# Optimization experiments

Hardware: AMD Instinct MI355X
Metric: run time of the kernel (lower is better)

Reference implementation:

```python
import jax, jax.numpy as jnp
import numpy as np

N_HOPS = 3
GAMMA = 0.2
N_CAP = 3  # self.N: hops < N use alpha, hop == N uses eta
EPS = 1e-8

N_USERS, N_ENT, N_KG_EDGES, N_INTER_EDGES, D, N_REL = 50000, 100000, 300000, 300000, 256, 21


def setup_inputs() -> dict:
    key = jax.random.key(0)
    ks = jax.random.split(key, 9)
    user_emb = jax.random.normal(ks[0], (N_USERS, D), jnp.float32) * 0.1
    entity_emb = jax.random.normal(ks[1], (N_ENT, D), jnp.float32) * 0.1
    edge_index = jax.random.randint(ks[2], (2, N_KG_EDGES), 0, N_ENT, dtype=jnp.int32)
    edge_type = jax.random.randint(ks[3], (N_KG_EDGES,), 1, N_REL, dtype=jnp.int32)  # 1-based relation ids
    omega = jax.random.uniform(ks[4], (N_KG_EDGES,), jnp.float32)
    inter_u = jax.random.randint(ks[5], (N_INTER_EDGES,), 0, N_USERS, dtype=jnp.int32)
    inter_i = jax.random.randint(ks[6], (N_INTER_EDGES,), 0, N_ENT, dtype=jnp.int32)
    inter_edge = jnp.stack([inter_u, inter_i])
    inter_edge_w = jax.random.uniform(ks[7], (N_INTER_EDGES,), jnp.float32)
    relation_emb = jax.random.normal(ks[8], (N_REL - 1, D), jnp.float32) * 0.1  # xavier-like
    return {
        "user_emb": user_emb,
        "entity_emb": entity_emb,
        "edge_index": edge_index,
        "edge_type": edge_type,
        "omega": omega,
        "inter_edge": inter_edge,
        "inter_edge_w": inter_edge_w,
        "relation_emb": relation_emb,
    }


def _l2norm(x):
    # F.normalize(x, dim=-1, eps=1e-8): x / max(||x||_2, eps)
    n = jnp.sqrt(jnp.sum(x * x, axis=-1, keepdims=True))
    return x / jnp.maximum(n, EPS)


def _clean(x):
    return jnp.nan_to_num(x, nan=0.0, posinf=10000.0, neginf=0.0001)


def reference(user_emb, entity_emb, edge_index, edge_type, omega, inter_edge, inter_edge_w, relation_emb):
    head, tail = edge_index[0], edge_index[1]
    E = omega.shape[0]
    n_ent = entity_emb.shape[0]
    n_users = user_emb.shape[0]

    # alpha/eta depend only on omega & head (constant across hops) -> hoist out of the hop loop
    denom = jax.ops.segment_sum(omega, head, num_segments=E)[head] + EPS
    alpha = omega / denom
    eta0 = jnp.where(alpha > GAMMA, alpha, 0.0)
    eta = eta0 / (jax.ops.segment_sum(eta0, head, num_segments=E)[head] + EPS)

    rel = relation_emb[edge_type - 1]  # [E, D]
    cnt = jnp.maximum(jax.ops.segment_sum(jnp.ones((E,), entity_emb.dtype), head, num_segments=n_ent), 1.0)

    ent_res, usr_res = entity_emb, user_emb
    ent, usr = entity_emb, user_emb
    for i in range(N_HOPS):
        hop = i + 1
        rho = alpha if hop < N_CAP else eta
        msg = rho[:, None] * (ent[tail] * rel)                       # [E, D]
        ent_agg = jax.ops.segment_sum(msg, head, num_segments=n_ent) / cnt[:, None]  # scatter_mean
        item_agg = inter_edge_w[:, None] * ent[inter_edge[1]]        # [IE, D]
        usr_agg = jax.ops.segment_sum(item_agg, inter_edge[0], num_segments=n_users)  # scatter_sum
        ent = _clean(_l2norm(ent_agg))
        usr = _clean(_l2norm(usr_agg))
        ent_res = ent_res + ent
        usr_res = usr_res + usr
    return (ent_res, usr_res)
```

## Files before the change

### kernel.cpp

```cpp
#include <hip/hip_runtime.h>
#include <math.h>

#define D 256
#define EPSV 1e-8f
#define GAMMAV 0.2f
#define SCAN_B 256

__device__ __forceinline__ float cleanf(float x) {
    if (isnan(x)) return 0.0f;
    if (isinf(x)) return x > 0.0f ? 10000.0f : 0.0001f;
    return x;
}

__device__ __forceinline__ unsigned short f2bf(float x) {
    unsigned u = __float_as_uint(x);
    return (unsigned short)((u + 0x7FFFu + ((u >> 16) & 1u)) >> 16);
}
__device__ __forceinline__ float bf2f(unsigned short b) {
    return __uint_as_float(((unsigned)b) << 16);
}


__global__ __launch_bounds__(256) void k_pre(
    const float4* __restrict__ ein, ushort4* __restrict__ eout, int n4, int nbc,
    const int* __restrict__ head, const float* __restrict__ omega,
    const int* __restrict__ iu,
    int* __restrict__ counts_e, int* __restrict__ counts_u,
    float* __restrict__ denom, int E, int IE) {
    if ((int)blockIdx.x < nbc) {
        int i = blockIdx.x * 256 + threadIdx.x;
        if (i < n4) {
            float4 v = ein[i];
            eout[i] = make_ushort4(f2bf(v.x), f2bf(v.y), f2bf(v.z), f2bf(v.w));
        }
    } else {
        int i = (blockIdx.x - nbc) * 256 + threadIdx.x;
        if (i < E) {
            int h = head[i];
            atomicAdd(&counts_e[h], 1);
            atomicAdd(&denom[h], omega[i]);
        } else if (i < E + IE) {
            atomicAdd(&counts_u[iu[i - E]], 1);
        }
    }
}


__global__ __launch_bounds__(SCAN_B) void k_scan1(
    const int* __restrict__ ce, int* __restrict__ oe, int* __restrict__ be,
    int nE, int nbE,
    const int* __restrict__ cu, int* __restrict__ ou, int* __restrict__ bu,
    int nU) {
    __shared__ int tmp[SCAN_B];
    const int* in; int* out; int* bs; int n; int lb;
    if ((int)blockIdx.x < nbE) { in = ce; out = oe; bs = be; n = nE; lb = blockIdx.x; }
    else { in = cu; out = ou; bs = bu; n = nU; lb = blockIdx.x - nbE; }
    int i = lb * SCAN_B + threadIdx.x;
    int v = (i < n) ? in[i] : 0;
    tmp[threadIdx.x] = v;
    __syncthreads();
    for (int o = 1; o < SCAN_B; o <<= 1) {
        int t = (threadIdx.x >= (unsigned)o) ? tmp[threadIdx.x - o] : 0;
        __syncthreads();
        tmp[threadIdx.x] += t;
        __syncthreads();
    }
    if (i < n) out[i] = tmp[threadIdx.x] - v;
    if (threadIdx.x == SCAN_B - 1) bs[lb] = tmp[threadIdx.x];
}

__global__ __launch_bounds__(1024) void k_scan2(
    int* __restrict__ be, int nbE, int* __restrict__ bu, int nbU) {
    __shared__ int tmp[1024];
    int* bs = (blockIdx.x == 0) ? be : bu;
    int nb  = (blockIdx.x == 0) ? nbE : nbU;
    int v = ((int)threadIdx.x < nb) ? bs[threadIdx.x] : 0;
    tmp[threadIdx.x] = v;
    __syncthreads();
    for (int o = 1; o < 1024; o <<= 1) {
        int t = (threadIdx.x >= (unsigned)o) ? tmp[threadIdx.x - o] : 0;
        __syncthreads();
        tmp[threadIdx.x] += t;
        __syncthreads();
    }
    if ((int)threadIdx.x < nb) bs[threadIdx.x] = tmp[threadIdx.x] - v;
}

__global__ __launch_bounds__(SCAN_B) void k_scan3(
    int* __restrict__ oe, int* __restrict__ cure, const int* __restrict__ be,
    int nE, int nbE,
    int* __restrict__ ou, int* __restrict__ curu, const int* __restrict__ bu,
    int nU) {
    int* out; int* cur; const int* bs; int n; int lb;
    if ((int)blockIdx.x < nbE) { out = oe; cur = cure; bs = be; n = nE; lb = blockIdx.x; }
    else { out = ou; cur = curu; bs = bu; n = nU; lb = blockIdx.x - nbE; }
    int i = lb * SCAN_B + threadIdx.x;
    if (i < n) {
        int v = out[i] + bs[lb];
        out[i] = v;
        cur[i] = v;
    }
}


__global__ __launch_bounds__(256) void k_fill_both(
    const int* __restrict__ head, const int* __restrict__ tail,
    const int* __restrict__ etype, const float* __restrict__ omega,
    const int* __restrict__ iu, const int* __restrict__ ii,
    const float* __restrict__ iw,
    const float* __restrict__ denom, float* __restrict__ denom2,
    int* __restrict__ cursor_e, int* __restrict__ cursor_u,
    int2* __restrict__ kg, int2* __restrict__ uc, int E, int IE) {
    int i = blockIdx.x * blockDim.x + threadIdx.x;
    if (i < E) {
        int h = head[i];
        float a = omega[i] / (denom[h] + EPSV);
        int p = atomicAdd(&cursor_e[h], 1);
        int2 m;
        m.x = tail[i] | ((etype[i] - 1) << 20);
        m.y = __float_as_int(a);
        kg[p] = m;
        if (a > GAMMAV) atomicAdd(&denom2[h], a);
    } else if (i < E + IE) {
        int e = i - E;
        int u = iu[e];
        int p = atomicAdd(&cursor_u[u], 1);
        int2 m;
        m.x = ii[e];
        m.y = __float_as_int(iw[e]);
        uc[p] = m;
    }
}


__global__ __launch_bounds__(256) void k_hop(
    const int* __restrict__ offs_e, const int* __restrict__ cnt_e,
    const int2* __restrict__ kg,
    const int* __restrict__ offs_u, const int* __restrict__ cnt_u,
    const int2* __restrict__ uc,
    const float* __restrict__ denom2,
    const float* __restrict__ rel,
    const unsigned short* __restrict__ src,
    const unsigned short* __restrict__ ent0b,
    const unsigned short* __restrict__ y1b,
    const unsigned short* __restrict__ y2b,
    unsigned short* __restrict__ ent_out_b,
    float* __restrict__ ent_res,
    const float* __restrict__ user0,
    float* __restrict__ usr_res,
    int n_ent, int n_users, int hop) {
    int row  = (int)((blockIdx.x * (size_t)blockDim.x + threadIdx.x) >> 6);
    int lane = threadIdx.x & 63;
    if (row < n_ent) {
        int s = offs_e[row], deg = cnt_e[row];
        int end = s + deg;
        const bool eta = (hop == 3);
        float den2i = 0.0f;
        if (eta) den2i = 1.0f / (denom2[row] + EPSV);
        float4 acc = make_float4(0.f, 0.f, 0.f, 0.f);
        for (int j = s; j < end; j += 4) {
            int e1 = end - 1;
            int2 mm[4];
            #pragma unroll
            for (int k = 0; k < 4; ++k) {
                int jj = j + k;
                mm[k] = kg[jj < end ? jj : e1];
            }
            ushort4 eb[4];
            float4  rw[4];
            float   rv[4];
            #pragma unroll
            for (int k = 0; k < 4; ++k) {
                int t = mm[k].x & 0xFFFFF;
                int r = ((unsigned)mm[k].x) >> 20;
                float a = __int_as_float(mm[k].y);
                float x = a;
                if (eta) x = (a > GAMMAV) ? a * den2i : 0.0f;
                rv[k] = (j + k < end) ? x : 0.0f;
                eb[k] = ((const ushort4*)(src + (size_t)t * D))[lane];
                rw[k] = ((const float4*)(rel + (size_t)r * D))[lane];
            }
            #pragma unroll
            for (int k = 0; k < 4; ++k) {
                acc.x += rv[k] * bf2f(eb[k].x) * rw[k].x;
                acc.y += rv[k] * bf2f(eb[k].y) * rw[k].y;
                acc.z += rv[k] * bf2f(eb[k].z) * rw[k].z;
                acc.w += rv[k] * bf2f(eb[k].w) * rw[k].w;
            }
        }
        float cinv = 1.0f / ((deg > 0) ? (float)deg : 1.0f);
        acc.x *= cinv; acc.y *= cinv; acc.z *= cinv; acc.w *= cinv;
        float ss = acc.x * acc.x + acc.y * acc.y + acc.z * acc.z + acc.w * acc.w;
        #pragma unroll
        for (int o = 32; o >= 1; o >>= 1) ss += __shfl_down(ss, o);
        ss = __shfl(ss, 0);
        float nrm = sqrtf(ss);
        float dninv = 1.0f / ((nrm > EPSV) ? nrm : EPSV);
        float4 y;
        y.x = cleanf(acc.x * dninv);
        y.y = cleanf(acc.y * dninv);
        y.z = cleanf(acc.z * dninv);
        y.w = cleanf(acc.w * dninv);
        if (hop == 3) {
            ushort4 a0 = ((const ushort4*)(ent0b + (size_t)row * D))[lane];
            ushort4 a1 = ((const ushort4*)(y1b  + (size_t)row * D))[lane];
            ushort4 a2 = ((const ushort4*)(y2b  + (size_t)row * D))[lane];
            y.x += bf2f(a0.x) + bf2f(a1.x) + bf2f(a2.x);
            y.y += bf2f(a0.y) + bf2f(a1.y) + bf2f(a2.y);
            y.z += bf2f(a0.z) + bf2f(a1.z) + bf2f(a2.z);
            y.w += bf2f(a0.w) + bf2f(a1.w) + bf2f(a2.w);
            ((float4*)(ent_res + (size_t)row * D))[lane] = y;
        } else {
            ((ushort4*)(ent_out_b + (size_t)row * D))[lane] =
                make_ushort4(f2bf(y.x), f2bf(y.y), f2bf(y.z), f2bf(y.w));
        }
    } else {
        int u = row - n_ent;
        if (u >= n_users) return;
        int s = offs_u[u], deg = cnt_u[u];
        int end = s + deg;
        float4 acc = make_float4(0.f, 0.f, 0.f, 0.f);
        for (int j = s; j < end; j += 4) {
            int e1 = end - 1;
            int2 mm[4];
            #pragma unroll
            for (int k = 0; k < 4; ++k) {
                int jj = j + k;
                mm[k] = uc[jj < end ? jj : e1];
            }
            ushort4 eb[4];
            float   wv[4];
            #pragma unroll
            for (int k = 0; k < 4; ++k) {
                wv[k] = (j + k < end) ? __int_as_float(mm[k].y) : 0.0f;
                eb[k] = ((const ushort4*)(src + (size_t)mm[k].x * D))[lane];
            }
            #pragma unroll
            for (int k = 0; k < 4; ++k) {
                acc.x += wv[k] * bf2f(eb[k].x);
                acc.y += wv[k] * bf2f(eb[k].y);
                acc.z += wv[k] * bf2f(eb[k].z);
                acc.w += wv[k] * bf2f(eb[k].w);
            }
        }
        float ss = acc.x * acc.x + acc.y * acc.y + acc.z * acc.z + acc.w * acc.w;
        #pragma unroll
        for (int o = 32; o >= 1; o >>= 1) ss += __shfl_down(ss, o);
        ss = __shfl(ss, 0);
        float nrm = sqrtf(ss);
        float dninv = 1.0f / ((nrm > EPSV) ? nrm : EPSV);
        float4 y;
        y.x = cleanf(acc.x * dninv);
        y.y = cleanf(acc.y * dninv);
        y.z = cleanf(acc.z * dninv);
        y.w = cleanf(acc.w * dninv);
        float4 base;
        if (hop == 1) base = ((const float4*)(user0 + (size_t)u * D))[lane];
        else          base = ((const float4*)(usr_res + (size_t)u * D))[lane];
        y.x += base.x; y.y += base.y; y.z += base.z; y.w += base.w;
        ((float4*)(usr_res + (size_t)u * D))[lane] = y;
    }
}

extern "C" void kernel_launch(void* const* d_in, const int* in_sizes, int n_in,
                              void* d_out, int out_size, void* d_ws, size_t ws_size,
                              hipStream_t stream) {
    const float* user_emb   = (const float*)d_in[0];
    const float* entity_emb = (const float*)d_in[1];
    const int*   edge_index = (const int*)d_in[2];
    const int*   edge_type  = (const int*)d_in[3];
    const float* omega      = (const float*)d_in[4];
    const int*   inter_edge = (const int*)d_in[5];
    const float* inter_w    = (const float*)d_in[6];
    const float* rel_emb    = (const float*)d_in[7];

    const int n_users = in_sizes[0] / D;
    const int n_ent   = in_sizes[1] / D;
    const int E       = in_sizes[3];
    const int IE      = in_sizes[6];

    const int* head = edge_index;
    const int* tail = edge_index + E;
    const int* iu   = inter_edge;
    const int* ii   = inter_edge + IE;

    char* w = (char*)d_ws;
    size_t entBh = (size_t)n_ent * D * sizeof(unsigned short);
    unsigned short* ent0b = (unsigned short*)w;  w += entBh;
    unsigned short* ent_a = (unsigned short*)w;  w += entBh;
    unsigned short* ent_b = (unsigned short*)w;  w += entBh;
    int2*  kg    = (int2*)w;   w += (size_t)E * sizeof(int2);
    int2*  ucsr  = (int2*)w;   w += (size_t)IE * sizeof(int2);
    int*   counts_e = (int*)w;   w += (size_t)n_ent * sizeof(int);
    int*   counts_u = (int*)w;   w += (size_t)n_users * sizeof(int);
    float* denom    = (float*)w; w += (size_t)n_ent * sizeof(float);
    float* denom2   = (float*)w; w += (size_t)n_ent * sizeof(float);
    size_t zeroB = ((size_t)n_ent * 3 + n_users) * sizeof(int);
    int*   offs_e   = (int*)w; w += (size_t)n_ent * sizeof(int);
    int*   offs_u   = (int*)w; w += (size_t)n_users * sizeof(int);
    int*   cursor_e = (int*)w; w += (size_t)n_ent * sizeof(int);
    int*   cursor_u = (int*)w; w += (size_t)n_users * sizeof(int);
    int*   bsums_e  = (int*)w; w += 1024 * sizeof(int);
    int*   bsums_u  = (int*)w; w += 1024 * sizeof(int);

    float* ent_res = (float*)d_out;
    float* usr_res = (float*)d_out + (size_t)n_ent * D;

    hipMemsetAsync(counts_e, 0, zeroB, stream);

    int n4  = n_ent * (D / 4);
    int nbc = (n4 + 255) / 256;
    int total_edges = E + IE;
    int eb = (total_edges + 255) / 256;
    k_pre<<<nbc + eb, 256, 0, stream>>>(
        (const float4*)entity_emb, (ushort4*)ent0b, n4, nbc,
        head, omega, iu, counts_e, counts_u, denom, E, IE);

    int nbE = (n_ent + SCAN_B - 1) / SCAN_B;
    int nbU = (n_users + SCAN_B - 1) / SCAN_B;
    k_scan1<<<nbE + nbU, SCAN_B, 0, stream>>>(counts_e, offs_e, bsums_e, n_ent, nbE,
                                              counts_u, offs_u, bsums_u, n_users);
    k_scan2<<<2, 1024, 0, stream>>>(bsums_e, nbE, bsums_u, nbU);
    k_scan3<<<nbE + nbU, SCAN_B, 0, stream>>>(offs_e, cursor_e, bsums_e, n_ent, nbE,
                                              offs_u, cursor_u, bsums_u, n_users);

    k_fill_both<<<eb, 256, 0, stream>>>(head, tail, edge_type, omega, iu, ii,
                                        inter_w, denom, denom2,
                                        cursor_e, cursor_u, kg, ucsr, E, IE);

    size_t waves = (size_t)n_ent + n_users;
    int gb = (int)((waves * 64 + 255) / 256);

    k_hop<<<gb, 256, 0, stream>>>(offs_e, counts_e, kg, offs_u, counts_u, ucsr,
                                  denom2, rel_emb, ent0b, ent0b, ent_a, ent_b,
                                  ent_a, ent_res, user_emb, usr_res,
                                  n_ent, n_users, 1);
    k_hop<<<gb, 256, 0, stream>>>(offs_e, counts_e, kg, offs_u, counts_u, ucsr,
                                  denom2, rel_emb, ent_a, ent0b, ent_a, ent_b,
                                  ent_b, ent_res, user_emb, usr_res,
                                  n_ent, n_users, 2);
    k_hop<<<gb, 256, 0, stream>>>(offs_e, counts_e, kg, offs_u, counts_u, ucsr,
                                  denom2, rel_emb, ent_b, ent0b, ent_a, ent_b,
                                  ent_b , ent_res, user_emb, usr_res,
                                  n_ent, n_users, 3);
}
```

Before: 613.2 us.

## Merge scan kernels, pack CSR offset/count, and deepen gather loads in hop kernel

Replaces the three-kernel scan with one two-block scan kernel where each thread serially sums a contiguous chunk. Offsets and counts are packed into int2 so each row loads both with one access. In the hop kernel, residual and base loads are hoisted ahead of the gather loop, the user loop is unrolled to 8 gathers, and sched_barriers force all loads to issue before the FMAs. These aim to cut launch overhead and raise memory-level parallelism. The cost is a serial, poorly coalesced scan on only two blocks and higher register pressure.

Result: slower. 826.5 us (+34.8%).

```diff
diff --git a/kernel.cpp b/kernel.cpp
--- a/kernel.cpp
+++ b/kernel.cpp
@@ -4,7 +4,6 @@
 #define D 256
 #define EPSV 1e-8f
 #define GAMMAV 0.2f
-#define SCAN_B 256
 
 __device__ __forceinline__ float cleanf(float x) {
     if (isnan(x)) return 0.0f;
@@ -18,6 +17,24 @@
 }
 __device__ __forceinline__ float bf2f(unsigned short b) {
     return __uint_as_float(((unsigned)b) << 16);
+}
+
+__device__ __forceinline__ float ewgt(int bits, bool eta, float den2i) {
+    float a = __int_as_float(bits);
+    return eta ? ((a > GAMMAV) ? a * den2i : 0.0f) : a;
+}
+
+__device__ __forceinline__ void fma4(float4& acc, float w, ushort4 eb, float4 rw) {
+    acc.x += w * bf2f(eb.x) * rw.x;
+    acc.y += w * bf2f(eb.y) * rw.y;
+    acc.z += w * bf2f(eb.z) * rw.z;
+    acc.w += w * bf2f(eb.w) * rw.w;
+}
+__device__ __forceinline__ void fma4u(float4& acc, float w, ushort4 eb) {
+    acc.x += w * bf2f(eb.x);
+    acc.y += w * bf2f(eb.y);
+    acc.z += w * bf2f(eb.z);
+    acc.w += w * bf2f(eb.w);
 }
 
 
@@ -46,59 +63,33 @@
 }
 
 
-__global__ __launch_bounds__(SCAN_B) void k_scan1(
-    const int* __restrict__ ce, int* __restrict__ oe, int* __restrict__ be,
-    int nE, int nbE,
-    const int* __restrict__ cu, int* __restrict__ ou, int* __restrict__ bu,
-    int nU) {
-    __shared__ int tmp[SCAN_B];
-    const int* in; int* out; int* bs; int n; int lb;
-    if ((int)blockIdx.x < nbE) { in = ce; out = oe; bs = be; n = nE; lb = blockIdx.x; }
-    else { in = cu; out = ou; bs = bu; n = nU; lb = blockIdx.x - nbE; }
-    int i = lb * SCAN_B + threadIdx.x;
-    int v = (i < n) ? in[i] : 0;
-    tmp[threadIdx.x] = v;
-    __syncthreads();
-    for (int o = 1; o < SCAN_B; o <<= 1) {
-        int t = (threadIdx.x >= (unsigned)o) ? tmp[threadIdx.x - o] : 0;
-        __syncthreads();
-        tmp[threadIdx.x] += t;
-        __syncthreads();
-    }
-    if (i < n) out[i] = tmp[threadIdx.x] - v;
-    if (threadIdx.x == SCAN_B - 1) bs[lb] = tmp[threadIdx.x];
-}
-
-__global__ __launch_bounds__(1024) void k_scan2(
-    int* __restrict__ be, int nbE, int* __restrict__ bu, int nbU) {
+__global__ __launch_bounds__(1024) void k_scan(
+    const int* __restrict__ ce, int2* __restrict__ oce, int* __restrict__ cure, int nE,
+    const int* __restrict__ cu, int2* __restrict__ ocu, int* __restrict__ curu, int nU) {
+    const int* cnt; int2* oc; int* cur; int n;
+    if (blockIdx.x == 0) { cnt = ce; oc = oce; cur = cure; n = nE; }
+    else                 { cnt = cu; oc = ocu; cur = curu; n = nU; }
+    int per = (n + 1023) / 1024;
+    int t = threadIdx.x;
+    int s0 = t * per;
+    int s1 = s0 + per; if (s1 > n) s1 = n;
+    int sum = 0;
+    for (int i = s0; i < s1; ++i) sum += cnt[i];
     __shared__ int tmp[1024];
-    int* bs = (blockIdx.x == 0) ? be : bu;
-    int nb  = (blockIdx.x == 0) ? nbE : nbU;
-    int v = ((int)threadIdx.x < nb) ? bs[threadIdx.x] : 0;
-    tmp[threadIdx.x] = v;
+    tmp[t] = sum;
     __syncthreads();
     for (int o = 1; o < 1024; o <<= 1) {
-        int t = (threadIdx.x >= (unsigned)o) ? tmp[threadIdx.x - o] : 0;
+        int v = (t >= o) ? tmp[t - o] : 0;
         __syncthreads();
-        tmp[threadIdx.x] += t;
+        tmp[t] += v;
         __syncthreads();
     }
-    if ((int)threadIdx.x < nb) bs[threadIdx.x] = tmp[threadIdx.x] - v;
-}
-
-__global__ __launch_bounds__(SCAN_B) void k_scan3(
-    int* __restrict__ oe, int* __restrict__ cure, const int* __restrict__ be,
-    int nE, int nbE,
-    int* __restrict__ ou, int* __restrict__ curu, const int* __restrict__ bu,
-    int nU) {
-    int* out; int* cur; const int* bs; int n; int lb;
-    if ((int)blockIdx.x < nbE) { out = oe; cur = cure; bs = be; n = nE; lb = blockIdx.x; }
-    else { out = ou; cur = curu; bs = bu; n = nU; lb = blockIdx.x - nbE; }
-    int i = lb * SCAN_B + threadIdx.x;
-    if (i < n) {
-        int v = out[i] + bs[lb];
-        out[i] = v;
-        cur[i] = v;
+    int base = tmp[t] - sum;
+    for (int i = s0; i < s1; ++i) {
+        int c = cnt[i];
+        oc[i] = make_int2(base, c);
+        cur[i] = base;
+        base += c;
     }
 }
 
@@ -134,10 +125,8 @@
 
 
 __global__ __launch_bounds__(256) void k_hop(
-    const int* __restrict__ offs_e, const int* __restrict__ cnt_e,
-    const int2* __restrict__ kg,
-    const int* __restrict__ offs_u, const int* __restrict__ cnt_u,
-    const int2* __restrict__ uc,
+    const int2* __restrict__ oc_e, const int2* __restrict__ kg,
+    const int2* __restrict__ oc_u, const int2* __restrict__ uc,
     const float* __restrict__ denom2,
     const float* __restrict__ rel,
     const unsigned short* __restrict__ src,
@@ -151,42 +140,48 @@
     int n_ent, int n_users, int hop) {
     int row  = (int)((blockIdx.x * (size_t)blockDim.x + threadIdx.x) >> 6);
     int lane = threadIdx.x & 63;
+    const ushort4* srcv = (const ushort4*)src;
+    const float4*  relv = (const float4*)rel;
     if (row < n_ent) {
-        int s = offs_e[row], deg = cnt_e[row];
+        int2 oc = oc_e[row];
+        int s = oc.x, deg = oc.y;
         int end = s + deg;
         const bool eta = (hop == 3);
         float den2i = 0.0f;
-        if (eta) den2i = 1.0f / (denom2[row] + EPSV);
+        ushort4 a0, a1, a2;
+        if (eta) {
+            den2i = 1.0f / (denom2[row] + EPSV);
+            a0 = ((const ushort4*)ent0b)[row * 64 + lane];
+            a1 = ((const ushort4*)y1b )[row * 64 + lane];
+            a2 = ((const ushort4*)y2b )[row * 64 + lane];
+        }
         float4 acc = make_float4(0.f, 0.f, 0.f, 0.f);
         for (int j = s; j < end; j += 4) {
             int e1 = end - 1;
-            int2 mm[4];
-            #pragma unroll
-            for (int k = 0; k < 4; ++k) {
-                int jj = j + k;
-                mm[k] = kg[jj < end ? jj : e1];
-            }
-            ushort4 eb[4];
-            float4  rw[4];
-            float   rv[4];
-            #pragma unroll
-            for (int k = 0; k < 4; ++k) {
-                int t = mm[k].x & 0xFFFFF;
-                int r = ((unsigned)mm[k].x) >> 20;
-                float a = __int_as_float(mm[k].y);
-                float x = a;
-                if (eta) x = (a > GAMMAV) ? a * den2i : 0.0f;
-                rv[k] = (j + k < end) ? x : 0.0f;
-                eb[k] = ((const ushort4*)(src + (size_t)t * D))[lane];
-                rw[k] = ((const float4*)(rel + (size_t)r * D))[lane];
-            }
-            #pragma unroll
-            for (int k = 0; k < 4; ++k) {
-                acc.x += rv[k] * bf2f(eb[k].x) * rw[k].x;
-                acc.y += rv[k] * bf2f(eb[k].y) * rw[k].y;
-                acc.z += rv[k] * bf2f(eb[k].z) * rw[k].z;
-                acc.w += rv[k] * bf2f(eb[k].w) * rw[k].w;
-            }
+            int j1 = (j + 1 < end) ? j + 1 : e1;
+            int j2 = (j + 2 < end) ? j + 2 : e1;
+            int j3 = (j + 3 < end) ? j + 3 : e1;
+            int2 m0 = kg[j];
+            int2 m1 = kg[j1];
+            int2 m2 = kg[j2];
+            int2 m3 = kg[j3];
+            ushort4 eb0 = srcv[(m0.x & 0xFFFFF) * 64 + lane];
+            ushort4 eb1 = srcv[(m1.x & 0xFFFFF) * 64 + lane];
+            ushort4 eb2 = srcv[(m2.x & 0xFFFFF) * 64 + lane];
+            ushort4 eb3 = srcv[(m3.x & 0xFFFFF) * 64 + lane];
+            float4 rw0 = relv[(((unsigned)m0.x) >> 20) * 64 + lane];
+            float4 rw1 = relv[(((unsigned)m1.x) >> 20) * 64 + lane];
+            float4 rw2 = relv[(((unsigned)m2.x) >> 20) * 64 + lane];
+            float4 rw3 = relv[(((unsigned)m3.x) >> 20) * 64 + lane];
+            __builtin_amdgcn_sched_barrier(0);
+            float w0 = ewgt(m0.y, eta, den2i);
+            float w1 = (j + 1 < end) ? ewgt(m1.y, eta, den2i) : 0.0f;
+            float w2 = (j + 2 < end) ? ewgt(m2.y, eta, den2i) : 0.0f;
+            float w3 = (j + 3 < end) ? ewgt(m3.y, eta, den2i) : 0.0f;
+            fma4(acc, w0, eb0, rw0);
+            fma4(acc, w1, eb1, rw1);
+            fma4(acc, w2, eb2, rw2);
+            fma4(acc, w3, eb3, rw3);
         }
         float cinv = 1.0f / ((deg > 0) ? (float)deg : 1.0f);
         acc.x *= cinv; acc.y *= cinv; acc.z *= cinv; acc.w *= cinv;
@@ -202,9 +197,6 @@
         y.z = cleanf(acc.z * dninv);
         y.w = cleanf(acc.w * dninv);
         if (hop == 3) {
-            ushort4 a0 = ((const ushort4*)(ent0b + (size_t)row * D))[lane];
-            ushort4 a1 = ((const ushort4*)(y1b  + (size_t)row * D))[lane];
-            ushort4 a2 = ((const ushort4*)(y2b  + (size_t)row * D))[lane];
             y.x += bf2f(a0.x) + bf2f(a1.x) + bf2f(a2.x);
             y.y += bf2f(a0.y) + bf2f(a1.y) + bf2f(a2.y);
             y.z += bf2f(a0.z) + bf2f(a1.z) + bf2f(a2.z);
@@ -217,30 +209,30 @@
     } else {
         int u = row - n_ent;
         if (u >= n_users) return;
-        int s = offs_u[u], deg = cnt_u[u];
+        int2 oc = oc_u[u];
+        int s = oc.x, deg = oc.y;
         int end = s + deg;
+        float4 base;
+        if (hop == 1) base = ((const float4*)user0)[u * 64 + lane];
+        else          base = ((const float4*)usr_res)[u * 64 + lane];
         float4 acc = make_float4(0.f, 0.f, 0.f, 0.f);
-        for (int j = s; j < end; j += 4) {
+        for (int j = s; j < end; j += 8) {
             int e1 = end - 1;
-            int2 mm[4];
+            int2 mm[8];
             #pragma unroll
-            for (int k = 0; k < 4; ++k) {
+            for (int k = 0; k < 8; ++k) {
                 int jj = j + k;
                 mm[k] = uc[jj < end ? jj : e1];
             }
-            ushort4 eb[4];
-            float   wv[4];
+            ushort4 eb[8];
             #pragma unroll
-            for (int k = 0; k < 4; ++k) {
-                wv[k] = (j + k < end) ? __int_as_float(mm[k].y) : 0.0f;
-                eb[k] = ((const ushort4*)(src + (size_t)mm[k].x * D))[lane];
-            }
+            for (int k = 0; k < 8; ++k)
+                eb[k] = srcv[(mm[k].x) * 64 + lane];
+            __builtin_amdgcn_sched_barrier(0);
             #pragma unroll
-            for (int k = 0; k < 4; ++k) {
-                acc.x += wv[k] * bf2f(eb[k].x);
-                acc.y += wv[k] * bf2f(eb[k].y);
-                acc.z += wv[k] * bf2f(eb[k].z);
-                acc.w += wv[k] * bf2f(eb[k].w);
+            for (int k = 0; k < 8; ++k) {
+                float wv = (j + k < end) ? __int_as_float(mm[k].y) : 0.0f;
+                fma4u(acc, wv, eb[k]);
             }
         }
         float ss = acc.x * acc.x + acc.y * acc.y + acc.z * acc.z + acc.w * acc.w;
@@ -250,14 +242,10 @@
         float nrm = sqrtf(ss);
         float dninv = 1.0f / ((nrm > EPSV) ? nrm : EPSV);
         float4 y;
-        y.x = cleanf(acc.x * dninv);
-        y.y = cleanf(acc.y * dninv);
-        y.z = cleanf(acc.z * dninv);
-        y.w = cleanf(acc.w * dninv);
-        float4 base;
-        if (hop == 1) base = ((const float4*)(user0 + (size_t)u * D))[lane];
-        else          base = ((const float4*)(usr_res + (size_t)u * D))[lane];
-        y.x += base.x; y.y += base.y; y.z += base.z; y.w += base.w;
+        y.x = cleanf(acc.x * dninv) + base.x;
+        y.y = cleanf(acc.y * dninv) + base.y;
+        y.z = cleanf(acc.z * dninv) + base.z;
+        y.w = cleanf(acc.w * dninv) + base.w;
         ((float4*)(usr_res + (size_t)u * D))[lane] = y;
     }
 }
@@ -296,12 +284,10 @@
     float* denom    = (float*)w; w += (size_t)n_ent * sizeof(float);
     float* denom2   = (float*)w; w += (size_t)n_ent * sizeof(float);
     size_t zeroB = ((size_t)n_ent * 3 + n_users) * sizeof(int);
-    int*   offs_e   = (int*)w; w += (size_t)n_ent * sizeof(int);
-    int*   offs_u   = (int*)w; w += (size_t)n_users * sizeof(int);
+    int2*  oc_e     = (int2*)w; w += (size_t)n_ent * sizeof(int2);
+    int2*  oc_u     = (int2*)w; w += (size_t)n_users * sizeof(int2);
     int*   cursor_e = (int*)w; w += (size_t)n_ent * sizeof(int);
     int*   cursor_u = (int*)w; w += (size_t)n_users * sizeof(int);
-    int*   bsums_e  = (int*)w; w += 1024 * sizeof(int);
-    int*   bsums_u  = (int*)w; w += 1024 * sizeof(int);
 
     float* ent_res = (float*)d_out;
     float* usr_res = (float*)d_out + (size_t)n_ent * D;
@@ -316,13 +302,8 @@
         (const float4*)entity_emb, (ushort4*)ent0b, n4, nbc,
         head, omega, iu, counts_e, counts_u, denom, E, IE);
 
-    int nbE = (n_ent + SCAN_B - 1) / SCAN_B;
-    int nbU = (n_users + SCAN_B - 1) / SCAN_B;
-    k_scan1<<<nbE + nbU, SCAN_B, 0, stream>>>(counts_e, offs_e, bsums_e, n_ent, nbE,
-                                              counts_u, offs_u, bsums_u, n_users);
-    k_scan2<<<2, 1024, 0, stream>>>(bsums_e, nbE, bsums_u, nbU);
-    k_scan3<<<nbE + nbU, SCAN_B, 0, stream>>>(offs_e, cursor_e, bsums_e, n_ent, nbE,
-                                              offs_u, cursor_u, bsums_u, n_users);
+    k_scan<<<2, 1024, 0, stream>>>(counts_e, oc_e, cursor_e, n_ent,
+                                   counts_u, oc_u, cursor_u, n_users);
 
     k_fill_both<<<eb, 256, 0, stream>>>(head, tail, edge_type, omega, iu, ii,
                                         inter_w, denom, denom2,
@@ -331,15 +312,15 @@
     size_t waves = (size_t)n_ent + n_users;
     int gb = (int)((waves * 64 + 255) / 256);
 
-    k_hop<<<gb, 256, 0, stream>>>(offs_e, counts_e, kg, offs_u, counts_u, ucsr,
+    k_hop<<<gb, 256, 0, stream>>>(oc_e, kg, oc_u, ucsr,
                                   denom2, rel_emb, ent0b, ent0b, ent_a, ent_b,
                                   ent_a, ent_res, user_emb, usr_res,
                                   n_ent, n_users, 1);
-    k_hop<<<gb, 256, 0, stream>>>(offs_e, counts_e, kg, offs_u, counts_u, ucsr,
+    k_hop<<<gb, 256, 0, stream>>>(oc_e, kg, oc_u, ucsr,
                                   denom2, rel_emb, ent_a, ent0b, ent_a, ent_b,
                                   ent_b, ent_res, user_emb, usr_res,
                                   n_ent, n_users, 2);
-    k_hop<<<gb, 256, 0, stream>>>(offs_e, counts_e, kg, offs_u, counts_u, ucsr,
+    k_hop<<<gb, 256, 0, stream>>>(oc_e, kg, oc_u, ucsr,
                                   denom2, rel_emb, ent_b, ent0b, ent_a, ent_b,
                                   ent_b , ent_res, user_emb, usr_res,
                                   n_ent, n_users, 3);
```
